# Kernel tuning notes

Hardware: AMD Instinct MI355X
Metric: run time of the kernel (lower is better)

The kernel has to match this reference:

```python
import jax, jax.numpy as jnp
import numpy as np

DIM = 768
NUM_HEADS = 12
HEAD_DIM = DIM // NUM_HEADS
SCALE = HEAD_DIM ** -0.5


def setup_inputs() -> dict:
    key = jax.random.key(0)
    ks = jax.random.split(key, 12)
    B, N, C, H = 8, 1024, DIM, NUM_HEADS
    s = 0.02
    return {
        'q_in': jax.random.normal(ks[0], (B, N, C), jnp.float32),
        'kv_in': jax.random.normal(ks[1], (B, N, C), jnp.float32),
        'Wq': jax.random.normal(ks[2], (C, C), jnp.float32) * s,
        'Wk': jax.random.normal(ks[3], (C, C), jnp.float32) * s,
        'Wv': jax.random.normal(ks[4], (C, C), jnp.float32) * s,
        'Wp': jax.random.normal(ks[5], (C, C), jnp.float32) * s,
        'bp': jnp.zeros((C,), jnp.float32),
        'W_dy2': jax.random.normal(ks[6], (H, C), jnp.float32) * s,  # lf gate linear (out=H)
        'b_dy2': jnp.zeros((H,), jnp.float32),
        'W_dy': jax.random.normal(ks[7], (H, C), jnp.float32) * s,   # hf gate linear
        'b_dy': jnp.zeros((H,), jnp.float32),
        'lf_gamma': jnp.full((C,), 1e-5, jnp.float32),
        'hf_gamma': jnp.full((C,), 1e-5, jnp.float32),
        'star_scale': jnp.ones((1,), jnp.float32),
        'star_bias': jnp.zeros((1,), jnp.float32),
    }


def reference(q_in, kv_in, Wq, Wk, Wv, Wp, bp, W_dy2, b_dy2, W_dy, b_dy,
              lf_gamma, hf_gamma, star_scale, star_bias):
    B, Nq, C = q_in.shape
    Nk = kv_in.shape[1]
    H, D = NUM_HEADS, HEAD_DIM

    # StarReLU on query tokens (ignore_cls_token = 0)
    dy_feat = star_scale * jnp.square(jax.nn.relu(q_in)) + star_bias  # (B,Nq,C)

    # low-freq dynamic gate: tanh(linear) per head, repeated over head_dim
    dy_lf = jnp.tanh(jnp.einsum('bnc,hc->bnh', dy_feat, W_dy2) + b_dy2)  # (B,Nq,H)
    dy_lf = jnp.repeat(dy_lf, D, axis=-1)  # (B,Nq,C)

    # high-freq dynamic gate: rational-of-softplus^2
    dy = jax.nn.softplus(jnp.einsum('bnc,hc->bnh', dy_feat, W_dy) + b_dy)
    dy2 = jnp.square(dy)
    dy_hf = 2.0 * dy2 / (dy2 + 0.3678)
    dy_hf = jnp.repeat(dy_hf, D, axis=-1)  # (B,Nq,C)

    # projections (torch Linear: y = x @ W.T), split heads
    q = jnp.einsum('bnc,dc->bnd', q_in, Wq).reshape(B, Nq, H, D).transpose(0, 2, 1, 3)
    k = jnp.einsum('bnc,dc->bnd', kv_in, Wk).reshape(B, Nk, H, D).transpose(0, 2, 1, 3)
    v = jnp.einsum('bnc,dc->bnd', kv_in, Wv).reshape(B, Nk, H, D).transpose(0, 2, 1, 3)

    attn = jnp.einsum('bhqd,bhkd->bhqk', q * SCALE, k)
    attn = jax.nn.softmax(attn, axis=-1)
    x_attn = jnp.einsum('bhqk,bhkd->bhqd', attn, v)
    x_attn = x_attn.transpose(0, 2, 1, 3).reshape(B, Nq, C)

    # Nk == Nq branch: per-token residual high-frequency component
    v_reshape = v.transpose(0, 2, 1, 3).reshape(B, Nk, C)
    v_hf = v_reshape - x_attn

    x_attn = x_attn + x_attn * dy_lf * lf_gamma
    x_attn = x_attn + dy_hf * v_hf * hf_gamma

    out = jnp.einsum('bnc,dc->bnd', x_attn, Wp) + bp
    return out
```

## Files before the change

### kernel.cpp

```cpp
#include <hip/hip_runtime.h>
#include <hip/hip_bf16.h>
#include <stdint.h>

typedef unsigned short u16;
typedef unsigned int u32;
typedef unsigned long long u64;
typedef __attribute__((ext_vector_type(8))) short short8;
typedef __attribute__((ext_vector_type(4))) float f32x4;

#define LOG2E 1.44269504f

static __device__ __forceinline__ u16 f2bf(float f) {
    u32 x = __float_as_uint(f);
    u32 r = (x + 0x7FFFu + ((x >> 16) & 1u)) >> 16;
    return (u16)r;
}
static __device__ __forceinline__ float bf2f(u16 u) {
    return __uint_as_float(((u32)u) << 16);
}
static __device__ __forceinline__ u32 pk2(float lo, float hi) {
    __hip_bfloat162 t = __float22bfloat162_rn(float2{lo, hi});
    union { __hip_bfloat162 b; u32 u; } cv;
    cv.b = t;
    return cv.u;
}
static __device__ __forceinline__ float fexp2(float x) {
#if __has_builtin(__builtin_amdgcn_exp2f)
    return __builtin_amdgcn_exp2f(x);
#else
    return exp2f(x);
#endif
}

static __device__ __forceinline__ void g2l16(const void* g, void* l) {
    __builtin_amdgcn_global_load_lds((const __attribute__((address_space(1))) void*)g,
                                     (__attribute__((address_space(3))) void*)l, 16, 0, 0);
}

__global__ __launch_bounds__(256) void k_cvt_all(
    const float* __restrict__ q_in, const float* __restrict__ kv_in,
    const float* __restrict__ Wq, const float* __restrict__ Wk,
    const float* __restrict__ Wv, const float* __restrict__ Wp,
    const float* __restrict__ Wdy2, const float* __restrict__ Wdy,
    u16* __restrict__ qbf, u16* __restrict__ kvbf, u16* __restrict__ Wqb,
    u16* __restrict__ Wkb, u16* __restrict__ Wvb, u16* __restrict__ Wpb,
    u16* __restrict__ wgb) {
    int i = blockIdx.x * 256 + threadIdx.x;
    const float* src;
    u16* dst;
    int so, dofs;
    if (i < 786432) { src = q_in; dst = qbf; so = i; dofs = i; }
    else if (i < 1572864) { src = kv_in; dst = kvbf; so = i - 786432; dofs = so; }
    else if (i < 1646592) { src = Wq; dst = Wqb; so = i - 1572864; dofs = so; }
    else if (i < 1720320) { src = Wk; dst = Wkb; so = i - 1646592; dofs = so; }
    else if (i < 1794048) { src = Wv; dst = Wvb; so = i - 1720320; dofs = so; }
    else if (i < 1867776) { src = Wp; dst = Wpb; so = i - 1794048; dofs = so; }
    else if (i < 1870080) {
        int e = i - 1867776;
        dst = wgb; dofs = e;
        if (e < 1152) { src = Wdy2; so = e; }
        else { src = Wdy; so = e - 1152; }
    } else return;
    const float4* p = (const float4*)src + (size_t)so * 2;
    float4 a = p[0], b = p[1];
    short8 o;
    o[0] = f2bf(a.x); o[1] = f2bf(a.y); o[2] = f2bf(a.z); o[3] = f2bf(a.w);
    o[4] = f2bf(b.x); o[5] = f2bf(b.y); o[6] = f2bf(b.z); o[7] = f2bf(b.w);
    *((short8*)dst + dofs) = o;
}

__global__ __launch_bounds__(64) void k_gates(
    const u16* __restrict__ qbf, const u16* __restrict__ wgb,
    const float* __restrict__ bdy2, const float* __restrict__ bdy,
    const float* __restrict__ star_s, const float* __restrict__ star_b,
    float* __restrict__ glf, float* __restrict__ ghf) {
    int lane = threadIdx.x;
    int g = lane >> 4, c = lane & 15;
    int row0 = blockIdx.x * 16;
    float ss = star_s[0], sb = star_b[0];
    f32x4 acc[2];
    acc[0] = (f32x4){0.f, 0.f, 0.f, 0.f};
    acc[1] = (f32x4){0.f, 0.f, 0.f, 0.f};
    for (int t = 0; t < 24; ++t) {
        int k0 = t * 32;
        short8 x8 = *(const short8*)(qbf + (size_t)(row0 + c) * 768 + k0 + g * 8);
        float f[8];
#pragma unroll
        for (int j = 0; j < 8; ++j) {
            float x = fmaxf(bf2f((u16)x8[j]), 0.f);
            f[j] = ss * x * x + sb;
        }
        union { u32 u[4]; short8 s8; } au;
#pragma unroll
        for (int j = 0; j < 4; ++j) au.u[j] = pk2(f[2 * j], f[2 * j + 1]);
        short8 b0 = *(const short8*)(wgb + (size_t)c * 768 + k0 + g * 8);
        short8 b1 = (short8){0, 0, 0, 0, 0, 0, 0, 0};
        if (c < 8)
            b1 = *(const short8*)(wgb + (size_t)(16 + c) * 768 + k0 + g * 8);
        acc[0] = __builtin_amdgcn_mfma_f32_16x16x32_bf16(au.s8, b0, acc[0], 0, 0, 0);
        acc[1] = __builtin_amdgcn_mfma_f32_16x16x32_bf16(au.s8, b1, acc[1], 0, 0, 0);
    }
#pragma unroll
    for (int n = 0; n < 2; ++n)
#pragma unroll
        for (int r = 0; r < 4; ++r) {
            int token = row0 + g * 4 + r;
            int o = n * 16 + c;
            float v = acc[n][r];
            if (o < 12) {
                glf[(size_t)token * 12 + o] = tanhf(v + bdy2[o]);
            } else if (o < 24) {
                float x = v + bdy[o - 12];
                float sp = (x > 15.f) ? x : log1pf(expf(x));
                float d2 = sp * sp;
                ghf[(size_t)token * 12 + (o - 12)] = 2.f * d2 / (d2 + 0.3678f);
            }
        }
}

__device__ __forceinline__ void gemm_core(const u16* __restrict__ A,
                                          const u16* __restrict__ W, u16* As,
                                          u16* Bs, int rowA0, int rowB0,
                                          int lane, int w, int wm, int wn,
                                          f32x4 acc[4][4]) {
    int g = lane >> 4, c = lane & 15;
#pragma unroll
    for (int m = 0; m < 4; ++m)
#pragma unroll
        for (int n = 0; n < 4; ++n) acc[m][n] = (f32x4){0.f, 0.f, 0.f, 0.f};

    auto stage = [&](int buf, int k0) {
#pragma unroll
        for (int j = 0; j < 2; ++j) {
            int L = w * 128 + j * 64 + lane;
            int p = L >> 3, s8 = L & 7;
            int t2 = s8 ^ (p & 7);
            int row = 2 * p + (t2 >> 2);
            int chunk = t2 & 3;
            size_t go = (size_t)row * 768 + k0 + chunk * 8;
            g2l16(A + (size_t)rowA0 * 768 + go, As + buf * 4096 + L * 8);
            g2l16(W + (size_t)rowB0 * 768 + go, Bs + buf * 4096 + L * 8);
        }
    };

    stage(0, 0);
    stage(1, 32);
    int cur = 0, nxt = 2;
    for (int t = 0; t < 24; ++t) {
        if (t < 23) asm volatile("s_waitcnt vmcnt(4)" ::: "memory");
        else        asm volatile("s_waitcnt vmcnt(0)" ::: "memory");
        __builtin_amdgcn_s_barrier();
        if (t < 22) stage(nxt, (t + 2) * 32);
        short8 a[4], b[4];
#pragma unroll
        for (int m = 0; m < 4; ++m) {
            int row = wm * 64 + m * 16 + c;
            int off = (row >> 1) * 64 +
                      ((((row & 1) << 2) | g) ^ ((row >> 1) & 7)) * 8;
            a[m] = *(const short8*)(As + cur * 4096 + off);
        }
#pragma unroll
        for (int n = 0; n < 4; ++n) {
            int row = wn * 64 + n * 16 + c;
            int off = (row >> 1) * 64 +
                      ((((row & 1) << 2) | g) ^ ((row >> 1) & 7)) * 8;
            b[n] = *(const short8*)(Bs + cur * 4096 + off);
        }
        __builtin_amdgcn_s_setprio(1);
#pragma unroll
        for (int m = 0; m < 4; ++m)
#pragma unroll
            for (int n = 0; n < 4; ++n)
                acc[m][n] = __builtin_amdgcn_mfma_f32_16x16x32_bf16(
                    a[m], b[n], acc[m][n], 0, 0, 0);
        __builtin_amdgcn_s_setprio(0);
        cur = (cur == 2) ? 0 : cur + 1;
        nxt = (nxt == 2) ? 0 : nxt + 1;
    }
}

static __device__ __forceinline__ int park_wb(int row, int col) {
    return row * 256 + ((col * 2) ^ (((row >> 2) & 3) << 5));
}
static __device__ __forceinline__ int park_rb(int srow, int sch) {
    return srow * 256 + ((sch * 16) ^ (((srow >> 2) & 3) << 5));
}

__global__ __launch_bounds__(256, 3) void k_gemm_qkv(
    const u16* __restrict__ qbf, const u16* __restrict__ kvbf,
    const u16* __restrict__ Wqb, const u16* __restrict__ Wkb,
    const u16* __restrict__ Wvb, u16* __restrict__ Qb, u16* __restrict__ Kb,
    u16* __restrict__ VTg, u16* __restrict__ vlin) {
    __shared__ __align__(16) u16 smem[24576];
    u16* As = smem;
    u16* Bs = smem + 12288;
    int bid = blockIdx.x;
    int logical = (bid & 7) * 144 + (bid >> 3);
    int panel = logical / 18, sub = logical % 18;
    int type = sub / 6, tn = sub % 6;
    int tid = threadIdx.x, lane = tid & 63, w = tid >> 6;
    int g = lane >> 4, c = lane & 15;
    int wm = w >> 1, wn = w & 1;
    int rowA0 = panel * 128, rowB0 = tn * 128;
    const u16* A = (type == 0) ? qbf : kvbf;
    const u16* W = (type == 0) ? Wqb : (type == 1) ? Wkb : Wvb;

    f32x4 acc[4][4];
    gemm_core(A, W, As, Bs, rowA0, rowB0, lane, w, wm, wn, acc);
    __syncthreads();

    if (type < 2) {
        u16* dst = (type == 0) ? Qb : Kb;
        const float scl = (type == 0) ? (0.125f * LOG2E) : 1.0f;
#pragma unroll
        for (int m = 0; m < 4; ++m)
#pragma unroll
            for (int n = 0; n < 4; ++n)
#pragma unroll
                for (int r = 0; r < 4; ++r) {
                    int row = wm * 64 + m * 16 + g * 4 + r;
                    int col = wn * 64 + n * 16 + c;
                    *(u16*)((char*)smem + park_wb(row, col)) =
                        f2bf(acc[m][n][r] * scl);
                }
        __syncthreads();
#pragma unroll
        for (int j = 0; j < 8; ++j) {
            int idx = j * 256 + tid;
            int srow = idx >> 4, sch = idx & 15;
            short8 v = *(const short8*)((char*)smem + park_rb(srow, sch));
            int token = rowA0 + srow;
            int col0 = rowB0 + sch * 8;
            int bb = token >> 10, nn = token & 1023, hh = col0 >> 6,
                dd = col0 & 63;
            *(short8*)(dst + ((size_t)(bb * 12 + hh) << 16) + (nn << 6) + dd) = v;
        }
    } else {
#pragma unroll
        for (int m = 0; m < 4; ++m)
#pragma unroll
            for (int n = 0; n < 4; ++n)
#pragma unroll
                for (int r = 0; r < 4; ++r) {
                    int row = wm * 64 + m * 16 + g * 4 + r;
                    int col = wn * 64 + n * 16 + c;
                    *(u16*)((char*)smem + park_wb(row, col)) = f2bf(acc[m][n][r]);
                }
        __syncthreads();
#pragma unroll
        for (int j = 0; j < 8; ++j) {
            int idx = j * 256 + tid;
            int srow = idx >> 4, sch = idx & 15;
            short8 v = *(const short8*)((char*)smem + park_rb(srow, sch));
            *(short8*)(vlin + (size_t)(rowA0 + srow) * 768 + rowB0 + sch * 8) = v;
        }
        __syncthreads();
#pragma unroll
        for (int m = 0; m < 4; ++m)
#pragma unroll
            for (int n = 0; n < 4; ++n)
#pragma unroll
                for (int r = 0; r < 4; ++r) {
                    int rl = wm * 64 + m * 16 + g * 4 + r;
                    int cl = wn * 64 + n * 16 + c;
                    smem[cl * 128 + rl] = f2bf(acc[m][n][r]);
                }
        __syncthreads();
        int bb = rowA0 >> 10, nn0 = rowA0 & 1023;
#pragma unroll
        for (int j = 0; j < 8; ++j) {
            int idx = j * 256 + tid;
            int rT = idx >> 4, cc = idx & 15;
            int dout = rowB0 + rT, hh = dout >> 6, dd = dout & 63;
            const u16* srow = smem + rT * 128 + cc * 8;
            size_t robase = ((size_t)(bb * 12 + hh) * 64 + dd) * 1024;
#pragma unroll
            for (int e2 = 0; e2 < 4; ++e2) {
                int n0 = nn0 + cc * 8 + 2 * e2;
                int t6 = n0 & 63;
                int pos = (((t6 >> 1) & 1) << 5) | (((t6 >> 2) & 3) << 3) |
                          (((t6 >> 4) & 3) << 1) | (t6 & 1);
                u32 val = (u32)srow[2 * e2] | ((u32)srow[2 * e2 + 1] << 16);
                *(u32*)(VTg + robase + (n0 & ~63) + pos) = val;
            }
        }
    }
}

__global__ __launch_bounds__(256, 3) void k_gemm_out(
    const u16* __restrict__ xf, const u16* __restrict__ Wpb,
    const float* __restrict__ bp, float* __restrict__ out) {
    __shared__ __align__(16) u16 smem[24576];
    u16* As = smem;
    u16* Bs = smem + 12288;
    int bid = blockIdx.x;
    int logical = (bid & 7) * 48 + (bid >> 3);
    int c48 = logical % 48;
    int tm = (logical / 48) * 8 + c48 / 6, tn = c48 % 6;
    int tid = threadIdx.x, lane = tid & 63, w = tid >> 6;
    int g = lane >> 4, c = lane & 15;
    int wm = w >> 1, wn = w & 1;
    int rowA0 = tm * 128, rowB0 = tn * 128;

    f32x4 acc[4][4];
    gemm_core(xf, Wpb, As, Bs, rowA0, rowB0, lane, w, wm, wn, acc);

    float bias[4];
#pragma unroll
    for (int n = 0; n < 4; ++n) bias[n] = bp[rowB0 + wn * 64 + n * 16 + c];

    char* F = (char*)smem;
#pragma unroll
    for (int p = 0; p < 2; ++p) {
        __syncthreads();
        if (wm == p) {
#pragma unroll
            for (int m = 0; m < 4; ++m)
#pragma unroll
                for (int n = 0; n < 4; ++n)
#pragma unroll
                    for (int r = 0; r < 4; ++r) {
                        int lrow = m * 16 + g * 4 + r;
                        int col = wn * 64 + n * 16 + c;
                        int byte = lrow * 512 +
                                   ((col * 4) ^ (((lrow >> 2) & 3) << 6));
                        *(float*)(F + byte) = acc[m][n][r] + bias[n];
                    }
        }
        __syncthreads();
#pragma unroll
        for (int j = 0; j < 8; ++j) {
            int idx = j * 256 + tid;
            int srow = idx >> 5, sch = idx & 31;
            int byte = srow * 512 + ((sch * 16) ^ (((srow >> 2) & 3) << 6));
            float4 v = *(const float4*)(F + byte);
            *(float4*)(out + (size_t)(rowA0 + p * 64 + srow) * 768 + rowB0 +
                       sch * 4) = v;
        }
    }
}

__global__ __launch_bounds__(256, 3) void k_attn(
    const u16* __restrict__ Qb, const u16* __restrict__ Kb,
    const u16* __restrict__ VTg, const u16* __restrict__ vlin,
    const float* __restrict__ glf, const float* __restrict__ ghf,
    const float* __restrict__ lfg, const float* __restrict__ hfg,
    u16* __restrict__ xfinal) {
    __shared__ __align__(16) u16 Ks[12288];
    __shared__ __align__(16) u16 Vs[12288];
    int b8 = blockIdx.x;
    int sw = (b8 & 7) * 96 + (b8 >> 3);
    int bh = sw >> 3, qblk = sw & 7;
    int bb = bh / 12, hh = bh % 12;
    int tid = threadIdx.x, lane = tid & 63, w = tid >> 6;
    int g = lane >> 4, c = lane & 15;
    const char* Kp = (const char*)(Kb + ((size_t)bh << 16));
    const char* Vp = (const char*)(VTg + ((size_t)bh << 16));
    const u16* Qp = Qb + ((size_t)bh << 16);
    int q0 = qblk * 128 + w * 32;

    short8 qf[2][2];
#pragma unroll
    for (int qb = 0; qb < 2; ++qb)
#pragma unroll
        for (int ks = 0; ks < 2; ++ks)
            qf[qb][ks] = *(const short8*)(Qp + (size_t)(q0 + qb * 16 + c) * 64 +
                                          ks * 32 + g * 8);

    f32x4 o[2][4];
#pragma unroll
    for (int qb = 0; qb < 2; ++qb)
#pragma unroll
        for (int n = 0; n < 4; ++n) o[qb][n] = (f32x4){0.f, 0.f, 0.f, 0.f};
    f32x4 o5[2];
    o5[0] = (f32x4){0.f, 0.f, 0.f, 0.f};
    o5[1] = (f32x4){0.f, 0.f, 0.f, 0.f};
    const short8 vones = (short8){(short)0x3F80, (short)0x3F80, (short)0x3F80,
                                  (short)0x3F80, (short)0x3F80, (short)0x3F80,
                                  (short)0x3F80, (short)0x3F80};

    int kgo[2], vgo[2], ldo[2];
#pragma unroll
    for (int h = 0; h < 2; ++h) {
        int idx = w * 64 + lane + h * 256;
        int row = idx >> 3;
        int colb = ((idx & 7) * 16) ^ ((row & 7) << 4);
        kgo[h] = row * 128 + colb;
        vgo[h] = row * 2048 + colb;
        ldo[h] = (w * 64 + h * 256) * 16;
    }

    auto stage = [&](int bi, int t) {
#pragma unroll
        for (int h = 0; h < 2; ++h) {
            g2l16(Kp + (size_t)t * 8192 + kgo[h], (char*)Ks + bi * 8192 + ldo[h]);
            g2l16(Vp + (size_t)t * 128 + vgo[h], (char*)Vs + bi * 8192 + ldo[h]);
        }
    };

    stage(0, 0);
    stage(1, 1);
    int cur = 0, nxt = 2;
    int cs = (c & 7) << 4;
    for (int t = 0; t < 16; ++t) {
        if (t < 15) asm volatile("s_waitcnt vmcnt(4)" ::: "memory");
        else        asm volatile("s_waitcnt vmcnt(0)" ::: "memory");
        __builtin_amdgcn_s_barrier();
        if (t < 14) stage(nxt, t + 2);
        const char* Kbase = (const char*)Ks + cur * 8192;
        const char* Vbase = (const char*)Vs + cur * 8192;
        short8 kf[4][2], vf[4][2];
#pragma unroll
        for (int m = 0; m < 4; ++m) {
            int rowb = (m * 16 + c) * 128;
#pragma unroll
            for (int ks = 0; ks < 2; ++ks)
                kf[m][ks] = *(const short8*)(Kbase + rowb +
                                             ((g * 16 + ks * 64) ^ cs));
        }
#pragma unroll
        for (int n = 0; n < 4; ++n) {
            int rowb = (n * 16 + c) * 128;
#pragma unroll
            for (int a = 0; a < 2; ++a)
                vf[n][a] = *(const short8*)(Vbase + rowb +
                                            ((a * 64 + g * 16) ^ cs));
        }
#pragma unroll
        for (int qb = 0; qb < 2; ++qb) {
            f32x4 s[4];
            __builtin_amdgcn_s_setprio(1);
#pragma unroll
            for (int m = 0; m < 4; ++m) {
                s[m] = __builtin_amdgcn_mfma_f32_16x16x32_bf16(
                    kf[m][0], qf[qb][0], (f32x4){0.f, 0.f, 0.f, 0.f}, 0, 0, 0);
                s[m] = __builtin_amdgcn_mfma_f32_16x16x32_bf16(
                    kf[m][1], qf[qb][1], s[m], 0, 0, 0);
            }
            __builtin_amdgcn_s_setprio(0);
            u32 P2[4][2];
#pragma unroll
            for (int m = 0; m < 4; ++m) {
#pragma unroll
                for (int r = 0; r < 4; ++r) s[m][r] = fexp2(s[m][r]);
                P2[m][0] = pk2(s[m][0], s[m][1]);
                P2[m][1] = pk2(s[m][2], s[m][3]);
            }
#pragma unroll
            for (int a = 0; a < 2; ++a) {
                union { u32 u[4]; short8 s8; } pu;
                pu.u[0] = P2[0][a]; pu.u[1] = P2[1][a];
                pu.u[2] = P2[2][a]; pu.u[3] = P2[3][a];
                __builtin_amdgcn_s_setprio(1);
#pragma unroll
                for (int n = 0; n < 4; ++n)
                    o[qb][n] = __builtin_amdgcn_mfma_f32_16x16x32_bf16(
                        pu.s8, vf[n][a], o[qb][n], 0, 0, 0);
                o5[qb] = __builtin_amdgcn_mfma_f32_16x16x32_bf16(
                    pu.s8, vones, o5[qb], 0, 0, 0);
                __builtin_amdgcn_s_setprio(0);
            }
        }
        cur = (cur == 2) ? 0 : cur + 1;
        nxt = (nxt == 2) ? 0 : nxt + 1;
    }
    __syncthreads();

    u16* X = &Ks[0];
#pragma unroll
    for (int qb = 0; qb < 2; ++qb) {
        float rl[4];
#pragma unroll
        for (int r = 0; r < 4; ++r) rl[r] = 1.0f / o5[qb][r];
#pragma unroll
        for (int n = 0; n < 4; ++n)
#pragma unroll
            for (int r = 0; r < 4; ++r) {
                int row = w * 32 + qb * 16 + 4 * g + r;
                int col = n * 16 + c;
                int byte = row * 128 + ((col * 2) ^ ((row & 3) << 4));
                *(u16*)((char*)X + byte) = f2bf(o[qb][n][r] * rl[r]);
            }
    }
    __syncthreads();
    {
        int row = tid >> 1, half = tid & 1;
        size_t token = (size_t)bb * 1024 + qblk * 128 + row;
        float alf = glf[token * 12 + hh];
        float ahf = ghf[token * 12 + hh];
        int dbase = hh * 64 + half * 32;
        const u16* vbase = vlin + token * 768 + dbase;
        u16* obase = xfinal + token * 768 + dbase;
#pragma unroll
        for (int j = 0; j < 4; ++j) {
            int phys = ((half * 4 + j) ^ (row & 3)) * 16;
            short8 xa8 = *(const short8*)((char*)X + row * 128 + phys);
            short8 vl8 = *(const short8*)(vbase + j * 8);
            float4 lg0 = *(const float4*)(lfg + dbase + j * 8);
            float4 lg1 = *(const float4*)(lfg + dbase + j * 8 + 4);
            float4 hg0 = *(const float4*)(hfg + dbase + j * 8);
            float4 hg1 = *(const float4*)(hfg + dbase + j * 8 + 4);
            float lg[8] = {lg0.x, lg0.y, lg0.z, lg0.w, lg1.x, lg1.y, lg1.z, lg1.w};
            float hg[8] = {hg0.x, hg0.y, hg0.z, hg0.w, hg1.x, hg1.y, hg1.z, hg1.w};
            short8 oo;
#pragma unroll
            for (int e = 0; e < 8; ++e) {
                float xa = bf2f((u16)xa8[e]);
                float v = bf2f((u16)vl8[e]);
                float val = xa + xa * alf * lg[e] + ahf * (v - xa) * hg[e];
                oo[e] = f2bf(val);
            }
            *(short8*)(obase + j * 8) = oo;
        }
    }
}

extern "C" void kernel_launch(void* const* d_in, const int* in_sizes, int n_in,
                              void* d_out, int out_size, void* d_ws,
                              size_t ws_size, hipStream_t stream) {
    const float* q_in = (const float*)d_in[0];
    const float* kv_in = (const float*)d_in[1];
    const float* Wq = (const float*)d_in[2];
    const float* Wk = (const float*)d_in[3];
    const float* Wv = (const float*)d_in[4];
    const float* Wp = (const float*)d_in[5];
    const float* bp = (const float*)d_in[6];
    const float* Wdy2 = (const float*)d_in[7];
    const float* bdy2 = (const float*)d_in[8];
    const float* Wdy = (const float*)d_in[9];
    const float* bdy = (const float*)d_in[10];
    const float* lfg = (const float*)d_in[11];
    const float* hfg = (const float*)d_in[12];
    const float* st_s = (const float*)d_in[13];
    const float* st_b = (const float*)d_in[14];
    float* out = (float*)d_out;

    char* ws = (char*)d_ws;
    const size_t MC2 = (size_t)8192 * 768 * 2;
    const size_t WB = (size_t)768 * 768 * 2;
    u16* qbf = (u16*)(ws);
    u16* kvbf = (u16*)(ws + MC2);
    u16* Wqb = (u16*)(ws + 2 * MC2);
    u16* Wkb = (u16*)(ws + 2 * MC2 + WB);
    u16* Wvb = (u16*)(ws + 2 * MC2 + 2 * WB);
    u16* Wpb = (u16*)(ws + 2 * MC2 + 3 * WB);
    u16* Qb = (u16*)(ws + 2 * MC2 + 4 * WB);
    u16* Kb = (u16*)(ws + 3 * MC2 + 4 * WB);
    u16* VTg = (u16*)(ws + 4 * MC2 + 4 * WB);
    u16* vlin = (u16*)(ws + 5 * MC2 + 4 * WB);
    float* glf = (float*)(ws + 6 * MC2 + 4 * WB);
    float* ghf = (float*)(ws + 6 * MC2 + 4 * WB + (size_t)8192 * 12 * 4);
    u16* wgb = (u16*)(ws + 6 * MC2 + 4 * WB + (size_t)8192 * 12 * 8);
    u16* xfinal = qbf;

    k_cvt_all<<<7305, 256, 0, stream>>>(q_in, kv_in, Wq, Wk, Wv, Wp, Wdy2,
                                        Wdy, qbf, kvbf, Wqb, Wkb, Wvb, Wpb,
                                        wgb);
    k_gates<<<512, 64, 0, stream>>>(qbf, wgb, bdy2, bdy, st_s, st_b, glf, ghf);
    k_gemm_qkv<<<1152, 256, 0, stream>>>(qbf, kvbf, Wqb, Wkb, Wvb, Qb, Kb,
                                         VTg, vlin);
    k_attn<<<768, 256, 0, stream>>>(Qb, Kb, VTg, vlin, glf, ghf, lfg, hfg,
                                    xfinal);
    k_gemm_out<<<384, 256, 0, stream>>>(xfinal, Wpb, bp, out);
}
```

Before: 133.7 us.

## Switch GEMM and attention pipelines to double buffering and raise occupancy to four

```diff
diff --git a/kernel.cpp b/kernel.cpp
--- a/kernel.cpp
+++ b/kernel.cpp
@@ -70,7 +70,7 @@
 }
 
 __global__ __launch_bounds__(64) void k_gates(
-    const u16* __restrict__ qbf, const u16* __restrict__ wgb,
+    const float* __restrict__ qin, const u16* __restrict__ wgb,
     const float* __restrict__ bdy2, const float* __restrict__ bdy,
     const float* __restrict__ star_s, const float* __restrict__ star_b,
     float* __restrict__ glf, float* __restrict__ ghf) {
@@ -83,11 +83,13 @@
     acc[1] = (f32x4){0.f, 0.f, 0.f, 0.f};
     for (int t = 0; t < 24; ++t) {
         int k0 = t * 32;
-        short8 x8 = *(const short8*)(qbf + (size_t)(row0 + c) * 768 + k0 + g * 8);
-        float f[8];
+        const float* qrow = qin + (size_t)(row0 + c) * 768 + k0 + g * 8;
+        float4 xa = *(const float4*)qrow;
+        float4 xb = *(const float4*)(qrow + 4);
+        float f[8] = {xa.x, xa.y, xa.z, xa.w, xb.x, xb.y, xb.z, xb.w};
 #pragma unroll
         for (int j = 0; j < 8; ++j) {
-            float x = fmaxf(bf2f((u16)x8[j]), 0.f);
+            float x = fmaxf(f[j], 0.f);
             f[j] = ss * x * x + sb;
         }
         union { u32 u[4]; short8 s8; } au;
@@ -118,6 +120,13 @@
         }
 }
 
+static __device__ __forceinline__ int park_wb(int row, int col) {
+    return row * 256 + ((col * 2) ^ (((row >> 2) & 3) << 5));
+}
+static __device__ __forceinline__ int park_rb(int srow, int sch) {
+    return srow * 256 + ((sch * 16) ^ (((srow >> 2) & 3) << 5));
+}
+
 __device__ __forceinline__ void gemm_core(const u16* __restrict__ A,
                                           const u16* __restrict__ W, u16* As,
                                           u16* Bs, int rowA0, int rowB0,
@@ -144,27 +153,29 @@
     };
 
     stage(0, 0);
-    stage(1, 32);
-    int cur = 0, nxt = 2;
+    int buf = 0;
     for (int t = 0; t < 24; ++t) {
-        if (t < 23) asm volatile("s_waitcnt vmcnt(4)" ::: "memory");
-        else        asm volatile("s_waitcnt vmcnt(0)" ::: "memory");
+        if (t < 23) {
+            stage(buf ^ 1, (t + 1) * 32);
+            asm volatile("s_waitcnt vmcnt(4)" ::: "memory");
+        } else {
+            asm volatile("s_waitcnt vmcnt(0)" ::: "memory");
+        }
         __builtin_amdgcn_s_barrier();
-        if (t < 22) stage(nxt, (t + 2) * 32);
         short8 a[4], b[4];
 #pragma unroll
         for (int m = 0; m < 4; ++m) {
             int row = wm * 64 + m * 16 + c;
             int off = (row >> 1) * 64 +
                       ((((row & 1) << 2) | g) ^ ((row >> 1) & 7)) * 8;
-            a[m] = *(const short8*)(As + cur * 4096 + off);
+            a[m] = *(const short8*)(As + buf * 4096 + off);
         }
 #pragma unroll
         for (int n = 0; n < 4; ++n) {
             int row = wn * 64 + n * 16 + c;
             int off = (row >> 1) * 64 +
                       ((((row & 1) << 2) | g) ^ ((row >> 1) & 7)) * 8;
-            b[n] = *(const short8*)(Bs + cur * 4096 + off);
+            b[n] = *(const short8*)(Bs + buf * 4096 + off);
         }
         __builtin_amdgcn_s_setprio(1);
 #pragma unroll
@@ -174,26 +185,19 @@
                 acc[m][n] = __builtin_amdgcn_mfma_f32_16x16x32_bf16(
                     a[m], b[n], acc[m][n], 0, 0, 0);
         __builtin_amdgcn_s_setprio(0);
-        cur = (cur == 2) ? 0 : cur + 1;
-        nxt = (nxt == 2) ? 0 : nxt + 1;
-    }
-}
-
-static __device__ __forceinline__ int park_wb(int row, int col) {
-    return row * 256 + ((col * 2) ^ (((row >> 2) & 3) << 5));
-}
-static __device__ __forceinline__ int park_rb(int srow, int sch) {
-    return srow * 256 + ((sch * 16) ^ (((srow >> 2) & 3) << 5));
-}
-
-__global__ __launch_bounds__(256, 3) void k_gemm_qkv(
+        __builtin_amdgcn_s_barrier();
+        buf ^= 1;
+    }
+}
+
+__global__ __launch_bounds__(256, 4) void k_gemm_qkv(
     const u16* __restrict__ qbf, const u16* __restrict__ kvbf,
     const u16* __restrict__ Wqb, const u16* __restrict__ Wkb,
     const u16* __restrict__ Wvb, u16* __restrict__ Qb, u16* __restrict__ Kb,
     u16* __restrict__ VTg, u16* __restrict__ vlin) {
-    __shared__ __align__(16) u16 smem[24576];
+    __shared__ __align__(16) u16 smem[16384];
     u16* As = smem;
-    u16* Bs = smem + 12288;
+    u16* Bs = smem + 8192;
     int bid = blockIdx.x;
     int logical = (bid & 7) * 144 + (bid >> 3);
     int panel = logical / 18, sub = logical % 18;
@@ -287,12 +291,12 @@
     }
 }
 
-__global__ __launch_bounds__(256, 3) void k_gemm_out(
+__global__ __launch_bounds__(256, 4) void k_gemm_out(
     const u16* __restrict__ xf, const u16* __restrict__ Wpb,
     const float* __restrict__ bp, float* __restrict__ out) {
-    __shared__ __align__(16) u16 smem[24576];
+    __shared__ __align__(16) u16 smem[16384];
     u16* As = smem;
-    u16* Bs = smem + 12288;
+    u16* Bs = smem + 8192;
     int bid = blockIdx.x;
     int logical = (bid & 7) * 48 + (bid >> 3);
     int c48 = logical % 48;
@@ -340,14 +344,14 @@
     }
 }
 
-__global__ __launch_bounds__(256, 3) void k_attn(
+__global__ __launch_bounds__(256, 4) void k_attn(
     const u16* __restrict__ Qb, const u16* __restrict__ Kb,
     const u16* __restrict__ VTg, const u16* __restrict__ vlin,
     const float* __restrict__ glf, const float* __restrict__ ghf,
     const float* __restrict__ lfg, const float* __restrict__ hfg,
     u16* __restrict__ xfinal) {
-    __shared__ __align__(16) u16 Ks[12288];
-    __shared__ __align__(16) u16 Vs[12288];
+    __shared__ __align__(16) u16 Ks[8192];
+    __shared__ __align__(16) u16 Vs[8192];
     int b8 = blockIdx.x;
     int sw = (b8 & 7) * 96 + (b8 >> 3);
     int bh = sw >> 3, qblk = sw & 7;
@@ -399,16 +403,18 @@
     };
 
     stage(0, 0);
-    stage(1, 1);
-    int cur = 0, nxt = 2;
+    int buf = 0;
     int cs = (c & 7) << 4;
     for (int t = 0; t < 16; ++t) {
-        if (t < 15) asm volatile("s_waitcnt vmcnt(4)" ::: "memory");
-        else        asm volatile("s_waitcnt vmcnt(0)" ::: "memory");
+        if (t < 15) {
+            stage(buf ^ 1, t + 1);
+            asm volatile("s_waitcnt vmcnt(4)" ::: "memory");
+        } else {
+            asm volatile("s_waitcnt vmcnt(0)" ::: "memory");
+        }
         __builtin_amdgcn_s_barrier();
-        if (t < 14) stage(nxt, t + 2);
-        const char* Kbase = (const char*)Ks + cur * 8192;
-        const char* Vbase = (const char*)Vs + cur * 8192;
+        const char* Kbase = (const char*)Ks + buf * 8192;
+        const char* Vbase = (const char*)Vs + buf * 8192;
         short8 kf[4][2], vf[4][2];
 #pragma unroll
         for (int m = 0; m < 4; ++m) {
@@ -461,8 +467,8 @@
                 __builtin_amdgcn_s_setprio(0);
             }
         }
-        cur = (cur == 2) ? 0 : cur + 1;
-        nxt = (nxt == 2) ? 0 : nxt + 1;
+        __builtin_amdgcn_s_barrier();
+        buf ^= 1;
     }
     __syncthreads();
 
@@ -556,7 +562,8 @@
     k_cvt_all<<<7305, 256, 0, stream>>>(q_in, kv_in, Wq, Wk, Wv, Wp, Wdy2,
                                         Wdy, qbf, kvbf, Wqb, Wkb, Wvb, Wpb,
                                         wgb);
-    k_gates<<<512, 64, 0, stream>>>(qbf, wgb, bdy2, bdy, st_s, st_b, glf, ghf);
+    k_gates<<<512, 64, 0, stream>>>(q_in, wgb, bdy2, bdy, st_s, st_b, glf,
+                                    ghf);
     k_gemm_qkv<<<1152, 256, 0, stream>>>(qbf, kvbf, Wqb, Wkb, Wvb, Qb, Kb,
                                          VTg, vlin);
     k_attn<<<768, 256, 0, stream>>>(Qb, Kb, VTg, vlin, glf, ghf, lfg, hfg,
```

New measurement: 182.6 us. 36.5% more time.
